# Optimization experiments

Hardware: AMD Instinct MI355X
Metric: run time of the kernel (lower is better)

The kernel has to match this reference:

```python
import jax, jax.numpy as jnp
import numpy as np

N = 50_000      # nodes
E = 800_000     # edges
IN_NF = 16      # input/output node feature dim
H = 64          # hidden_nf
NB = 2          # n_layers (EquivariantBlocks)
NG = 2          # inv_sublayers (GCLs per block)
NORM_FACTOR = 100.0
NORM_CONST = 1.0
EDGE_IN = 2 * H + 2  # edges_in_d = 2 (current + initial squared distance)


def setup_inputs() -> dict:
    key = jax.random.key(0)
    ks = iter(jax.random.split(key, 32))
    rn = lambda s: jax.random.normal(next(ks), s, dtype=jnp.float32)
    lin = lambda s: rn(s) / np.sqrt(s[-2]).astype(np.float32)  # ~xavier-ish
    inp = {
        'h': rn((N, IN_NF)),
        'x': rn((N, 3)),
        'row': jax.random.randint(next(ks), (E,), 0, N, dtype=jnp.int32),
        'col': jax.random.randint(next(ks), (E,), 0, N, dtype=jnp.int32),
        # embedding in/out
        'emb_w': lin((IN_NF, H)), 'emb_b': jnp.zeros((H,), jnp.float32),
        'out_w': lin((H, IN_NF)), 'out_b': jnp.zeros((IN_NF,), jnp.float32),
        # 4 GCLs total (NB*NG), stacked on leading axis
        'e_w1': lin((NB * NG, EDGE_IN, H)), 'e_b1': jnp.zeros((NB * NG, H), jnp.float32),
        'e_w2': lin((NB * NG, H, H)),       'e_b2': jnp.zeros((NB * NG, H), jnp.float32),
        'n_w1': lin((NB * NG, 2 * H, H)),   'n_b1': jnp.zeros((NB * NG, H), jnp.float32),
        'n_w2': lin((NB * NG, H, H)),       'n_b2': jnp.zeros((NB * NG, H), jnp.float32),
        # 2 EquivariantUpdates (one per block)
        'q_w1': lin((NB, EDGE_IN, H)), 'q_b1': jnp.zeros((NB, H), jnp.float32),
        'q_w2': lin((NB, H, H)),       'q_b2': jnp.zeros((NB, H), jnp.float32),
        'q_w3': lin((NB, H, 1)) * 0.001,  # xavier gain=0.001, no bias
    }
    return inp


def _egnn(h, x, row, col, emb_w, emb_b, out_w, out_b,
          e_w1, e_b1, e_w2, e_b2, n_w1, n_b1, n_w2, n_b2,
          q_w1, q_b1, q_w2, q_b2, q_w3):
    def coord2diff(xc):
        d = xc[row] - xc[col]                      # [E,3]
        radial = jnp.sum(d * d, axis=1, keepdims=True)  # [E,1]
        d = d / (jnp.sqrt(radial + 1e-8) + NORM_CONST)
        return radial, d

    dist0, _ = coord2diff(x)                       # initial distances, passed to every block
    h = h @ emb_w + emb_b
    for b in range(NB):
        radial, coord_diff = coord2diff(x)
        edge_attr = jnp.concatenate([radial, dist0], axis=1)  # [E,2]
        for i in range(NG):
            l = b * NG + i
            inp = jnp.concatenate([h[row], h[col], edge_attr], axis=1)  # [E, 2H+2]
            mij = jax.nn.silu(jax.nn.silu(inp @ e_w1[l] + e_b1[l]) @ e_w2[l] + e_b2[l])
            agg = jax.ops.segment_sum(mij, row, num_segments=N) / NORM_FACTOR
            node_in = jnp.concatenate([h, agg], axis=1)                 # [N, 2H]
            h = h + jax.nn.silu(node_in @ n_w1[l] + n_b1[l]) @ n_w2[l] + n_b2[l]
        # equivariant coordinate update
        inp = jnp.concatenate([h[row], h[col], edge_attr], axis=1)
        phi = jax.nn.silu(jax.nn.silu(inp @ q_w1[b] + q_b1[b]) @ q_w2[b] + q_b2[b]) @ q_w3[b]  # [E,1]
        trans = coord_diff * phi
        x = x + jax.ops.segment_sum(trans, row, num_segments=N) / NORM_FACTOR
    h = h @ out_w + out_b
    return h, x


def reference(h, x, row, col, emb_w, emb_b, out_w, out_b,
              e_w1, e_b1, e_w2, e_b2, n_w1, n_b1, n_w2, n_b2,
              q_w1, q_b1, q_w2, q_b2, q_w3):
    return _egnn(h, x, row, col, emb_w, emb_b, out_w, out_b,
                 e_w1, e_b1, e_w2, e_b2, n_w1, n_b1, n_w2, n_b2,
                 q_w1, q_b1, q_w2, q_b2, q_w3)
```

## Files before the change

kernel.cpp:

```cpp
#include <hip/hip_runtime.h>

#define NN 50000
#define NE 800000
#define NB 196

typedef unsigned int  u32;
typedef unsigned short u16;
typedef __attribute__((ext_vector_type(8))) short short8;
typedef __attribute__((ext_vector_type(4))) float f32x4;

union ABfrag { uint2 u2[2]; uint4 u4; short8 s8; };

__device__ __forceinline__ float silu_f(float v) {
    return v * __builtin_amdgcn_rcpf(1.0f + __expf(-v));
}
__device__ __forceinline__ u32 pk2(float lo, float hi) {
    return __builtin_amdgcn_perm(__float_as_uint(hi) + 0x8000u,
                                 __float_as_uint(lo) + 0x8000u, 0x07060302u);
}
__device__ __forceinline__ float bff(u32 h) { return __uint_as_float(h << 16); }

__global__ __launch_bounds__(256, 4) void k_embed(const float* __restrict__ h,
        const float* __restrict__ w, const float* __restrict__ b,
        float* __restrict__ h64) {
    int n = blockIdx.x * 256 + threadIdx.x;
    if (n >= NN) return;
    const float4* h4 = (const float4*)(h + (long)n * 16);
    float in[16];
    #pragma unroll
    for (int c = 0; c < 4; ++c) {
        float4 v = h4[c];
        in[4*c+0] = v.x; in[4*c+1] = v.y; in[4*c+2] = v.z; in[4*c+3] = v.w;
    }
    float acc[64];
    #pragma unroll
    for (int j = 0; j < 64; ++j) acc[j] = b[j];
    #pragma unroll
    for (int k = 0; k < 16; ++k) {
        #pragma unroll
        for (int j = 0; j < 64; ++j) acc[j] = fmaf(in[k], w[k*64 + j], acc[j]);
    }
    float4* o4 = (float4*)(h64 + (long)n * 64);
    #pragma unroll
    for (int c = 0; c < 16; ++c)
        o4[c] = make_float4(acc[4*c+0], acc[4*c+1], acc[4*c+2], acc[4*c+3]);
}

__global__ __launch_bounds__(256, 4) void k_hist(const int* __restrict__ row,
        int* __restrict__ deg) {
    int e = blockIdx.x * 256 + threadIdx.x;
    if (e < NE) atomicAdd(&deg[row[e]], 1);
}

__global__ __launch_bounds__(256, 4) void k_scanA(const int* __restrict__ deg,
        int* __restrict__ bsum) {
    int t = threadIdx.x, i = blockIdx.x * 256 + t;
    int v = (i < NN) ? deg[i] : 0;
    #pragma unroll
    for (int d = 1; d < 64; d <<= 1) v += __shfl_xor(v, d);
    __shared__ int ws[4];
    if ((t & 63) == 0) ws[t >> 6] = v;
    __syncthreads();
    if (t == 0) bsum[blockIdx.x] = ws[0] + ws[1] + ws[2] + ws[3];
}

__global__ __launch_bounds__(256) void k_scanB(const int* __restrict__ bsum,
        int* __restrict__ bpre) {
    __shared__ int s[256];
    int t = threadIdx.x;
    int v = (t < NB) ? bsum[t] : 0;
    s[t] = v;
    __syncthreads();
    #pragma unroll
    for (int d = 1; d < 256; d <<= 1) {
        int u = (t >= d) ? s[t - d] : 0;
        __syncthreads();
        s[t] += u;
        __syncthreads();
    }
    if (t < NB) bpre[t] = s[t] - v;
}

__global__ __launch_bounds__(256, 4) void k_scanC(const int* __restrict__ deg,
        const int* __restrict__ bpre, int* __restrict__ base) {
    int t = threadIdx.x, i = blockIdx.x * 256 + t;
    int lane = t & 63, w = t >> 6;
    int v = (i < NN) ? deg[i] : 0;
    int x = v;
    #pragma unroll
    for (int d = 1; d < 64; d <<= 1) {
        int u = __shfl_up(x, d);
        if (lane >= d) x += u;
    }
    __shared__ int wsum[4];
    if (lane == 63) wsum[w] = x;
    __syncthreads();
    int off = bpre[blockIdx.x];
    #pragma unroll
    for (int ww = 0; ww < 3; ++ww) if (ww < w) off += wsum[ww];
    if (i < NN) base[i] = off + x - v;
}

__global__ __launch_bounds__(256, 4) void k_scatter(const int* __restrict__ row,
        const int* __restrict__ col, int* __restrict__ base,
        int* __restrict__ rowS, int* __restrict__ colS) {
    int e = blockIdx.x * 256 + threadIdx.x;
    if (e >= NE) return;
    int r = row[e];
    int p = atomicAdd(&base[r], 1);
    rowS[p] = r;
    colS[p] = col[e];
}

__global__ __launch_bounds__(256, 4) void k_radial(const float* __restrict__ x,
        const int* __restrict__ rowS, const int* __restrict__ colS,
        float* __restrict__ radial) {
    int e = blockIdx.x * 256 + threadIdx.x;
    if (e >= NE) return;
    int r = rowS[e], c = colS[e];
    float dx = x[r*3+0] - x[c*3+0];
    float dy = x[r*3+1] - x[c*3+1];
    float dz = x[r*3+2] - x[c*3+2];
    radial[e] = dx*dx + dy*dy + dz*dz;
}

__device__ __forceinline__ u32 bfr_rne(float x) {
    u32 u = __float_as_uint(x);
    u += 0x7fffu + ((u >> 16) & 1u);
    return u >> 16;
}
__global__ __launch_bounds__(256, 4) void k_wconv(const float* __restrict__ e_w2,
        const float* __restrict__ q_w2, const float* __restrict__ n_w1,
        const float* __restrict__ n_w2, const float* __restrict__ e_w1,
        const float* __restrict__ q_w1, u16* __restrict__ wf) {
    int t = blockIdx.x * 256 + threadIdx.x;
    if (t >= 122880) return;
    int j, lane, n, s, k, col;
    if (t < 24576) {
        int L = t >> 12, v = t & 4095;
        j = v & 7; lane = (v >> 3) & 63; int ns = v >> 9; n = ns >> 1; s = ns & 1;
        k = 8*(lane >> 4) + j + 32*s;
        col = 16*n + (lane & 15);
        const float* src = (L < 4) ? e_w2 + (size_t)L*4096 : q_w2 + (size_t)(L-4)*4096;
        wf[t] = (u16)bfr_rne(src[k*64 + col]);
    } else if (t < 57344) {
        int u = t - 24576; int L = u >> 13, v = u & 8191;
        j = v & 7; lane = (v >> 3) & 63; int ns = v >> 9; n = ns >> 2; s = ns & 3;
        k = 8*(lane >> 4) + j + 32*s;
        col = 16*n + (lane & 15);
        wf[t] = (u16)bfr_rne(n_w1[(size_t)L*8192 + k*64 + col]);
    } else if (t < 73728) {
        int u = t - 57344; int L = u >> 12, v = u & 4095;
        j = v & 7; lane = (v >> 3) & 63; int ns = v >> 9; n = ns >> 1; s = ns & 1;
        k = 8*(lane >> 4) + j + 32*s;
        col = 16*n + (lane & 15);
        wf[t] = (u16)bfr_rne(n_w2[(size_t)L*4096 + k*64 + col]);
    } else {
        int u = t - 73728;
        int L = u >> 13;
        int v = u & 8191;
        int m = v >> 12;
        int v2 = v & 4095;
        j = v2 & 7; lane = (v2 >> 3) & 63; int ns = v2 >> 9; n = ns >> 1; s = ns & 1;
        k = 8*(lane >> 4) + j + 32*s;
        col = 16*n + (lane & 15);
        const float* src = (L < 4) ? e_w1 + (size_t)L*130*64
                                   : q_w1 + (size_t)(L-4)*130*64;
        wf[t] = (u16)bfr_rne(src[(size_t)(m*64 + k)*64 + col]);
    }
}

__global__ __launch_bounds__(256, 4) void k_pq(const float* __restrict__ h64,
        const u16* __restrict__ wpf, const float* __restrict__ b1,
        u32* __restrict__ Pb, u32* __restrict__ Qb) {
    __shared__ u16 A[64*64];
    __shared__ u16 XP[64*68], XQ[64*68];
    int t = threadIdx.x, w = t >> 6, lane = t & 63;
    int nb0 = blockIdx.x * 64;
    #pragma unroll
    for (int i = 0; i < 4; ++i) {
        int idx = i*256 + t;
        int r = idx >> 4, c = idx & 15;
        int n = nb0 + r;
        float4 v = make_float4(0.f, 0.f, 0.f, 0.f);
        if (n < NN) v = ((const float4*)(h64 + (size_t)n*64))[c];
        uint2 pk = make_uint2(pk2(v.x, v.y), pk2(v.z, v.w));
        *(uint2*)((char*)A + r*128 + ((8*c) ^ ((r & 15) << 3))) = pk;
    }
    __syncthreads();
    int r0 = lane & 15, g = lane >> 4;
    ABfrag bp[2], bq[2];
    #pragma unroll
    for (int s = 0; s < 2; ++s) {
        bp[s].u4 = *(const uint4*)(wpf + ((size_t)(w*2 + s)*64 + lane)*8);
        bq[s].u4 = *(const uint4*)(wpf + 4096 + ((size_t)(w*2 + s)*64 + lane)*8);
    }
    f32x4 aP[4], aQ[4];
    #pragma unroll
    for (int t4 = 0; t4 < 4; ++t4) {
        aP[t4] = (f32x4){0.f, 0.f, 0.f, 0.f};
        aQ[t4] = (f32x4){0.f, 0.f, 0.f, 0.f};
    }
    #pragma unroll
    for (int t4 = 0; t4 < 4; ++t4) {
        #pragma unroll
        for (int s = 0; s < 2; ++s) {
            int boff = 16*g + 64*s;
            ABfrag af;
            af.u2[0] = *(uint2*)((char*)A + (16*t4 + r0)*128 + ( boff      ^ (r0 << 3)));
            af.u2[1] = *(uint2*)((char*)A + (16*t4 + r0)*128 + ((boff + 8) ^ (r0 << 3)));
            aP[t4] = __builtin_amdgcn_mfma_f32_16x16x32_bf16(af.s8, bp[s].s8, aP[t4], 0, 0, 0);
            aQ[t4] = __builtin_amdgcn_mfma_f32_16x16x32_bf16(af.s8, bq[s].s8, aQ[t4], 0, 0, 0);
        }
    }
    float bv = b1[16*w + r0];
    #pragma unroll
    for (int t4 = 0; t4 < 4; ++t4)
        #pragma unroll
        for (int q = 0; q < 4; ++q) {
            int rw = 16*t4 + 4*g + q;
            XP[rw*68 + 16*w + r0] = (u16)(pk2(aP[t4][q] + bv, 0.f) & 0xffffu);
            XQ[rw*68 + 16*w + r0] = (u16)(pk2(aQ[t4][q], 0.f) & 0xffffu);
        }
    __syncthreads();
    int node = t >> 2, part = t & 3;
    if (nb0 + node < NN) {
        const u32* XPw = (const u32*)XP;
        const u32* XQw = (const u32*)XQ;
        u32 b[8];
        #pragma unroll
        for (int j = 0; j < 8; ++j) b[j] = XPw[node*34 + 8*part + j];
        uint4* dp = (uint4*)(Pb + (size_t)(nb0 + node)*32 + part*8);
        dp[0] = make_uint4(b[0], b[1], b[2], b[3]);
        dp[1] = make_uint4(b[4], b[5], b[6], b[7]);
        #pragma unroll
        for (int j = 0; j < 8; ++j) b[j] = XQw[node*34 + 8*part + j];
        uint4* dq = (uint4*)(Qb + (size_t)(nb0 + node)*32 + part*8);
        dq[0] = make_uint4(b[0], b[1], b[2], b[3]);
        dq[1] = make_uint4(b[4], b[5], b[6], b[7]);
    }
}

__global__ __launch_bounds__(256, 4) void k_edge(
        const u32* __restrict__ Pb, const u32* __restrict__ Qb,
        const float* __restrict__ radial, const float* __restrict__ dist0,
        const int* __restrict__ rowS, const int* __restrict__ colS,
        const float* __restrict__ w1t, const u16* __restrict__ w2f,
        const float* __restrict__ b2, float* __restrict__ agg) {
    __shared__ u16 S_lds[4][4224];
    int tid = threadIdx.x;
    int w = tid >> 6, lane = tid & 63;
    int e = blockIdx.x * 256 + w * 64 + lane;
    u16* Aw = S_lds[w];
    int r = rowS[e], c = colS[e];
    float rad = radial[e], d0 = dist0[e];
    const uint4* Pr = (const uint4*)(Pb + (size_t)r * 32);
    const uint4* Qc = (const uint4*)(Qb + (size_t)c * 32);
    int swz = (lane & 15) << 3;
    #pragma unroll
    for (int c8 = 0; c8 < 8; ++c8) {
        uint4 pu = Pr[c8], qu = Qc[c8];
        u32 pw[4] = {pu.x, pu.y, pu.z, pu.w};
        u32 qw[4] = {qu.x, qu.y, qu.z, qu.w};
        float hv[8];
        #pragma unroll
        for (int k2 = 0; k2 < 4; ++k2) {
            int f = 8*c8 + 2*k2;
            float pl = bff(pw[k2] & 0xffffu), ph = bff(pw[k2] >> 16);
            float ql = bff(qw[k2] & 0xffffu), qh = bff(qw[k2] >> 16);
            hv[2*k2]   = silu_f(pl + ql + rad*w1t[f]     + d0*w1t[64+f]);
            hv[2*k2+1] = silu_f(ph + qh + rad*w1t[f+1]   + d0*w1t[64+f+1]);
        }
        uint2 pkA = make_uint2(pk2(hv[0], hv[1]), pk2(hv[2], hv[3]));
        uint2 pkB = make_uint2(pk2(hv[4], hv[5]), pk2(hv[6], hv[7]));
        *(uint2*)((char*)Aw + lane*128 + ((16*c8)     ^ swz)) = pkA;
        *(uint2*)((char*)Aw + lane*128 + ((16*c8 + 8) ^ swz)) = pkB;
    }
    __syncthreads();
    ABfrag bf[4][2];
    #pragma unroll
    for (int n = 0; n < 4; ++n)
        #pragma unroll
        for (int s = 0; s < 2; ++s)
            bf[n][s].u4 = *(const uint4*)(w2f + ((n*2 + s)*64 + lane)*8);
    int r0 = lane & 15, g = lane >> 4;
    f32x4 acc[4][4];
    #pragma unroll
    for (int t = 0; t < 4; ++t)
        #pragma unroll
        for (int n = 0; n < 4; ++n)
            acc[t][n] = (f32x4){0.f, 0.f, 0.f, 0.f};
    #pragma unroll
    for (int t = 0; t < 4; ++t) {
        #pragma unroll
        for (int s = 0; s < 2; ++s) {
            int boff = 16*g + 64*s;
            ABfrag af;
            af.u2[0] = *(uint2*)((char*)Aw + (16*t + r0)*128 + ( boff      ^ (r0 << 3)));
            af.u2[1] = *(uint2*)((char*)Aw + (16*t + r0)*128 + ((boff + 8) ^ (r0 << 3)));
            #pragma unroll
            for (int n = 0; n < 4; ++n)
                acc[t][n] = __builtin_amdgcn_mfma_f32_16x16x32_bf16(
                    af.s8, bf[n][s].s8, acc[t][n], 0, 0, 0);
        }
    }
    __syncthreads();
    u16* Mw = Aw;
    #pragma unroll
    for (int n = 0; n < 4; ++n) {
        float b2v = b2[16*n + r0];
        #pragma unroll
        for (int t = 0; t < 4; ++t) {
            f32x4 z = acc[t][n];
            u32 p0 = pk2(silu_f(z[0] + b2v), silu_f(z[1] + b2v));
            u32 p1 = pk2(silu_f(z[2] + b2v), silu_f(z[3] + b2v));
            *(uint2*)((char*)Mw + (16*n + r0)*132 + 32*t + 8*g) = make_uint2(p0, p1);
        }
    }
    __syncthreads();
    int rnext = __shfl_down(r, 1);
    unsigned long long tm = __ballot((lane == 63) || (rnext != r));
    float racc = 0.0f;
    #pragma unroll
    for (int ch = 0; ch < 16; ++ch) {
        uint2 mm = *(uint2*)((char*)Mw + lane*132 + 8*ch);
        u32 mw[2] = {mm.x, mm.y};
        #pragma unroll
        for (int q = 0; q < 4; ++q) {
            int ee = 4*ch + q;
            racc += bff((mw[q >> 1] >> ((q & 1) * 16)) & 0xffffu);
            if ((tm >> ee) & 1ull) {
                int rr = __builtin_amdgcn_readlane(r, ee);
                atomicAdd(&agg[(size_t)rr*64 + lane], racc);
                racc = 0.0f;
            }
        }
    }
}

__global__ __launch_bounds__(256, 3) void k_node_pq(float* __restrict__ h64,
        const float* __restrict__ agg,
        const u16* __restrict__ w1f, const float* __restrict__ b1,
        const u16* __restrict__ w2f, const float* __restrict__ b2,
        const u16* __restrict__ wpf, const float* __restrict__ b1pq,
        u32* __restrict__ Pb, u32* __restrict__ Qb) {
    __shared__ u16 S[16512];
    u16* A0 = S;
    u16* A1 = S + 4096;
    u16* H  = S + 8192;
    u16* D  = S + 12288;
    u16* An = S;
    u16* XPh = S + 4096;
    u16* XQh = S + 8448;
    int t = threadIdx.x, w = t >> 6, lane = t & 63;
    int nb0 = blockIdx.x * 64;
    #pragma unroll
    for (int i = 0; i < 8; ++i) {
        int idx = i*256 + t;
        int r = idx >> 5, c = idx & 31;
        int n = nb0 + r;
        float4 v = make_float4(0.f, 0.f, 0.f, 0.f);
        if (n < NN) {
            if (c < 16) v = ((const float4*)(h64 + (size_t)n*64))[c];
            else {
                float4 a = ((const float4*)(agg + (size_t)n*64))[c-16];
                v = make_float4(a.x*0.01f, a.y*0.01f, a.z*0.01f, a.w*0.01f);
            }
        }
        uint2 pk = make_uint2(pk2(v.x, v.y), pk2(v.z, v.w));
        u16* dst = (c < 16) ? A0 : A1;
        int cc = c & 15;
        *(uint2*)((char*)dst + r*128 + ((8*cc) ^ ((r & 15) << 3))) = pk;
    }
    __syncthreads();
    int r0 = lane & 15, g = lane >> 4;
    ABfrag bf1[4];
    #pragma unroll
    for (int s = 0; s < 4; ++s)
        bf1[s].u4 = *(const uint4*)(w1f + ((size_t)(w*4 + s)*64 + lane)*8);
    f32x4 acc[4];
    #pragma unroll
    for (int t4 = 0; t4 < 4; ++t4) acc[t4] = (f32x4){0.f, 0.f, 0.f, 0.f};
    #pragma unroll
    for (int t4 = 0; t4 < 4; ++t4) {
        #pragma unroll
        for (int s = 0; s < 4; ++s) {
            const u16* Ah = (s < 2) ? A0 : A1;
            int boff = 16*g + 64*(s & 1);
            ABfrag af;
            af.u2[0] = *(uint2*)((char*)Ah + (16*t4 + r0)*128 + ( boff      ^ (r0 << 3)));
            af.u2[1] = *(uint2*)((char*)Ah + (16*t4 + r0)*128 + ((boff + 8) ^ (r0 << 3)));
            acc[t4] = __builtin_amdgcn_mfma_f32_16x16x32_bf16(
                af.s8, bf1[s].s8, acc[t4], 0, 0, 0);
        }
    }
    float b1v = b1[16*w + r0];
    #pragma unroll
    for (int t4 = 0; t4 < 4; ++t4)
        #pragma unroll
        for (int q = 0; q < 4; ++q) {
            int rw = 16*t4 + 4*g + q;
            u16 hv = (u16)(pk2(silu_f(acc[t4][q] + b1v), 0.f) & 0xffffu);
            *(u16*)((char*)H + rw*128 + ((2*(16*w + r0)) ^ ((rw & 15) << 3))) = hv;
        }
    __syncthreads();
    ABfrag bf2[2];
    #pragma unroll
    for (int s = 0; s < 2; ++s)
        bf2[s].u4 = *(const uint4*)(w2f + ((size_t)(w*2 + s)*64 + lane)*8);
    f32x4 acc2[4];
    #pragma unroll
    for (int t4 = 0; t4 < 4; ++t4) acc2[t4] = (f32x4){0.f, 0.f, 0.f, 0.f};
    #pragma unroll
    for (int t4 = 0; t4 < 4; ++t4) {
        #pragma unroll
        for (int s = 0; s < 2; ++s) {
            int boff = 16*g + 64*s;
            ABfrag af;
            af.u2[0] = *(uint2*)((char*)H + (16*t4 + r0)*128 + ( boff      ^ (r0 << 3)));
            af.u2[1] = *(uint2*)((char*)H + (16*t4 + r0)*128 + ((boff + 8) ^ (r0 << 3)));
            acc2[t4] = __builtin_amdgcn_mfma_f32_16x16x32_bf16(
                af.s8, bf2[s].s8, acc2[t4], 0, 0, 0);
        }
    }
    float b2v = b2[16*w + r0];
    #pragma unroll
    for (int t4 = 0; t4 < 4; ++t4)
        #pragma unroll
        for (int q = 0; q < 4; ++q) {
            int rw = 16*t4 + 4*g + q;
            D[rw*66 + 16*w + r0] = (u16)(pk2(acc2[t4][q] + b2v, 0.f) & 0xffffu);
        }
    __syncthreads();
    #pragma unroll
    for (int i = 0; i < 4; ++i) {
        int idx = i*256 + t;
        int rr = idx >> 4, cc = idx & 15;
        int n = nb0 + rr;
        float4 v = make_float4(0.f, 0.f, 0.f, 0.f);
        if (n < NN) {
            v = ((const float4*)(h64 + (size_t)n*64))[cc];
            v.x += bff(D[rr*66 + 4*cc + 0]);
            v.y += bff(D[rr*66 + 4*cc + 1]);
            v.z += bff(D[rr*66 + 4*cc + 2]);
            v.w += bff(D[rr*66 + 4*cc + 3]);
            ((float4*)(h64 + (size_t)n*64))[cc] = v;
        }
        uint2 pk = make_uint2(pk2(v.x, v.y), pk2(v.z, v.w));
        *(uint2*)((char*)An + rr*128 + ((8*cc) ^ ((rr & 15) << 3))) = pk;
    }
    __syncthreads();
    ABfrag bp[2], bq[2];
    #pragma unroll
    for (int s = 0; s < 2; ++s) {
        bp[s].u4 = *(const uint4*)(wpf + ((size_t)(w*2 + s)*64 + lane)*8);
        bq[s].u4 = *(const uint4*)(wpf + 4096 + ((size_t)(w*2 + s)*64 + lane)*8);
    }
    f32x4 aP[4], aQ[4];
    #pragma unroll
    for (int t4 = 0; t4 < 4; ++t4) {
        aP[t4] = (f32x4){0.f, 0.f, 0.f, 0.f};
        aQ[t4] = (f32x4){0.f, 0.f, 0.f, 0.f};
    }
    #pragma unroll
    for (int t4 = 0; t4 < 4; ++t4) {
        #pragma unroll
        for (int s = 0; s < 2; ++s) {
            int boff = 16*g + 64*s;
            ABfrag af;
            af.u2[0] = *(uint2*)((char*)An + (16*t4 + r0)*128 + ( boff      ^ (r0 << 3)));
            af.u2[1] = *(uint2*)((char*)An + (16*t4 + r0)*128 + ((boff + 8) ^ (r0 << 3)));
            aP[t4] = __builtin_amdgcn_mfma_f32_16x16x32_bf16(af.s8, bp[s].s8, aP[t4], 0, 0, 0);
            aQ[t4] = __builtin_amdgcn_mfma_f32_16x16x32_bf16(af.s8, bq[s].s8, aQ[t4], 0, 0, 0);
        }
    }
    float bv = b1pq[16*w + r0];
    #pragma unroll
    for (int t4 = 0; t4 < 4; ++t4)
        #pragma unroll
        for (int q = 0; q < 4; ++q) {
            int rw = 16*t4 + 4*g + q;
            XPh[rw*68 + 16*w + r0] = (u16)(pk2(aP[t4][q] + bv, 0.f) & 0xffffu);
            XQh[rw*68 + 16*w + r0] = (u16)(pk2(aQ[t4][q], 0.f) & 0xffffu);
        }
    __syncthreads();
    int node = t >> 2, part = t & 3;
    if (nb0 + node < NN) {
        const u32* XPw = (const u32*)XPh;
        const u32* XQw = (const u32*)XQh;
        u32 b[8];
        #pragma unroll
        for (int j = 0; j < 8; ++j) b[j] = XPw[node*34 + 8*part + j];
        uint4* dp = (uint4*)(Pb + (size_t)(nb0 + node)*32 + part*8);
        dp[0] = make_uint4(b[0], b[1], b[2], b[3]);
        dp[1] = make_uint4(b[4], b[5], b[6], b[7]);
        #pragma unroll
        for (int j = 0; j < 8; ++j) b[j] = XQw[node*34 + 8*part + j];
        uint4* dq = (uint4*)(Qb + (size_t)(nb0 + node)*32 + part*8);
        dq[0] = make_uint4(b[0], b[1], b[2], b[3]);
        dq[1] = make_uint4(b[4], b[5], b[6], b[7]);
    }
}

__global__ __launch_bounds__(256, 4) void k_coord(
        const u32* __restrict__ Pb, const u32* __restrict__ Qb,
        const float* __restrict__ radial, const float* __restrict__ dist0,
        const int* __restrict__ rowS, const int* __restrict__ colS,
        const float* __restrict__ w1t, const u16* __restrict__ w2f,
        const float* __restrict__ b2, const float* __restrict__ w3,
        const float* __restrict__ x_old, float* __restrict__ x_new) {
    __shared__ u16 A_lds[4][4096];
    int tid = threadIdx.x;
    int w = tid >> 6, lane = tid & 63;
    int e = blockIdx.x * 256 + w * 64 + lane;
    u16* Aw = A_lds[w];
    int r = rowS[e], c = colS[e];
    float rad = radial[e], d0 = dist0[e];
    const uint4* Pr = (const uint4*)(Pb + (size_t)r * 32);
    const uint4* Qc = (const uint4*)(Qb + (size_t)c * 32);
    int swz = (lane & 15) << 3;
    #pragma unroll
    for (int c8 = 0; c8 < 8; ++c8) {
        uint4 pu = Pr[c8], qu = Qc[c8];
        u32 pw[4] = {pu.x, pu.y, pu.z, pu.w};
        u32 qw[4] = {qu.x, qu.y, qu.z, qu.w};
        float hv[8];
        #pragma unroll
        for (int k2 = 0; k2 < 4; ++k2) {
            int f = 8*c8 + 2*k2;
            float pl = bff(pw[k2] & 0xffffu), ph = bff(pw[k2] >> 16);
            float ql = bff(qw[k2] & 0xffffu), qh = bff(qw[k2] >> 16);
            hv[2*k2]   = silu_f(pl + ql + rad*w1t[f]   + d0*w1t[64+f]);
            hv[2*k2+1] = silu_f(ph + qh + rad*w1t[f+1] + d0*w1t[64+f+1]);
        }
        uint2 pkA = make_uint2(pk2(hv[0], hv[1]), pk2(hv[2], hv[3]));
        uint2 pkB = make_uint2(pk2(hv[4], hv[5]), pk2(hv[6], hv[7]));
        *(uint2*)((char*)Aw + lane*128 + ((16*c8)     ^ swz)) = pkA;
        *(uint2*)((char*)Aw + lane*128 + ((16*c8 + 8) ^ swz)) = pkB;
    }
    __syncthreads();
    ABfrag bf[4][2];
    #pragma unroll
    for (int n = 0; n < 4; ++n)
        #pragma unroll
        for (int s = 0; s < 2; ++s)
            bf[n][s].u4 = *(const uint4*)(w2f + ((n*2 + s)*64 + lane)*8);
    int r0 = lane & 15, g = lane >> 4;
    f32x4 acc[4][4];
    #pragma unroll
    for (int t = 0; t < 4; ++t)
        #pragma unroll
        for (int n = 0; n < 4; ++n)
            acc[t][n] = (f32x4){0.f, 0.f, 0.f, 0.f};
    #pragma unroll
    for (int t = 0; t < 4; ++t) {
        #pragma unroll
        for (int s = 0; s < 2; ++s) {
            int boff = 16*g + 64*s;
            ABfrag af;
            af.u2[0] = *(uint2*)((char*)Aw + (16*t + r0)*128 + ( boff      ^ (r0 << 3)));
            af.u2[1] = *(uint2*)((char*)Aw + (16*t + r0)*128 + ((boff + 8) ^ (r0 << 3)));
            #pragma unroll
            for (int n = 0; n < 4; ++n)
                acc[t][n] = __builtin_amdgcn_mfma_f32_16x16x32_bf16(
                    af.s8, bf[n][s].s8, acc[t][n], 0, 0, 0);
        }
    }
    float w3v[4], b2v[4];
    #pragma unroll
    for (int n = 0; n < 4; ++n) { w3v[n] = w3[16*n + r0]; b2v[n] = b2[16*n + r0]; }
    float ph[16];
    #pragma unroll
    for (int t = 0; t < 4; ++t)
        #pragma unroll
        for (int q = 0; q < 4; ++q) {
            float s = 0.f;
            #pragma unroll
            for (int n = 0; n < 4; ++n)
                s = fmaf(silu_f(acc[t][n][q] + b2v[n]), w3v[n], s);
            ph[t*4 + q] = s;
        }
    __syncthreads();
    float* Mw = (float*)Aw;
    #pragma unroll
    for (int t4 = 0; t4 < 4; ++t4)
        #pragma unroll
        for (int q = 0; q < 4; ++q)
            Mw[(16*t4 + 4*g + q)*17 + r0] = ph[t4*4 + q];
    __syncthreads();
    float phi = 0.f;
    #pragma unroll
    for (int i = 0; i < 16; ++i) phi += Mw[lane*17 + i];
    phi *= 0.01f;
    float dx = x_old[r*3+0] - x_old[c*3+0];
    float dy = x_old[r*3+1] - x_old[c*3+1];
    float dz = x_old[r*3+2] - x_old[c*3+2];
    float inv = phi / (sqrtf(rad + 1e-8f) + 1.0f);
    float tx = dx * inv, ty = dy * inv, tz = dz * inv;
    int rprev = __shfl_up(r, 1);
    bool head = (lane == 0) || (rprev != r);
    unsigned long long hm = __ballot(head);
    int runid = __popcll(hm & ((2ull << lane) - 1ull));
    #pragma unroll
    for (int d = 1; d < 64; d <<= 1) {
        float ox = __shfl_up(tx, d);
        float oy = __shfl_up(ty, d);
        float oz = __shfl_up(tz, d);
        int orid = __shfl_up(runid, d);
        if (lane >= d && orid == runid) { tx += ox; ty += oy; tz += oz; }
    }
    int rid_next = __shfl_down(runid, 1);
    bool tail = (lane == 63) || (rid_next != runid);
    if (tail) {
        atomicAdd(&x_new[r*3+0], tx);
        atomicAdd(&x_new[r*3+1], ty);
        atomicAdd(&x_new[r*3+2], tz);
    }
}

__global__ __launch_bounds__(256, 4) void k_out(const float* __restrict__ h64,
        const float* __restrict__ w, const float* __restrict__ b,
        float* __restrict__ out) {
    int n = blockIdx.x * 256 + threadIdx.x;
    if (n >= NN) return;
    float acc[16];
    #pragma unroll
    for (int j = 0; j < 16; ++j) acc[j] = b[j];
    const float4* h4 = (const float4*)(h64 + (long)n*64);
    #pragma unroll
    for (int c = 0; c < 16; ++c) {
        float4 v = h4[c];
        float vv[4] = {v.x, v.y, v.z, v.w};
        #pragma unroll
        for (int t = 0; t < 4; ++t) {
            #pragma unroll
            for (int j = 0; j < 16; ++j)
                acc[j] = fmaf(vv[t], w[(4*c+t)*16 + j], acc[j]);
        }
    }
    float4* o4 = (float4*)(out + (long)n*16);
    #pragma unroll
    for (int cq = 0; cq < 4; ++cq)
        o4[cq] = make_float4(acc[4*cq+0],acc[4*cq+1],acc[4*cq+2],acc[4*cq+3]);
}

extern "C" void kernel_launch(void* const* d_in, const int* in_sizes, int n_in,
                              void* d_out, int out_size, void* d_ws, size_t ws_size,
                              hipStream_t stream) {
    const float* h_in  = (const float*)d_in[0];
    const float* x_in  = (const float*)d_in[1];
    const int*   row   = (const int*)d_in[2];
    const int*   col   = (const int*)d_in[3];
    const float* emb_w = (const float*)d_in[4];
    const float* emb_b = (const float*)d_in[5];
    const float* out_w = (const float*)d_in[6];
    const float* out_b = (const float*)d_in[7];
    const float* e_w1  = (const float*)d_in[8];
    const float* e_b1  = (const float*)d_in[9];
    const float* e_w2  = (const float*)d_in[10];
    const float* e_b2  = (const float*)d_in[11];
    const float* n_w1  = (const float*)d_in[12];
    const float* n_b1  = (const float*)d_in[13];
    const float* n_w2  = (const float*)d_in[14];
    const float* n_b2  = (const float*)d_in[15];
    const float* q_w1  = (const float*)d_in[16];
    const float* q_b1  = (const float*)d_in[17];
    const float* q_w2  = (const float*)d_in[18];
    const float* q_b2  = (const float*)d_in[19];
    const float* q_w3  = (const float*)d_in[20];

    const size_t WF_N = 122880;
    const size_t WF_BYTES = WF_N * sizeof(u16);
    size_t need = WF_BYTES + ((size_t)NN*64*4 + (size_t)NE*2 + (size_t)NN*3
                   + (size_t)NE*2 + (size_t)NN*2 + 1024) * sizeof(float);
    if (ws_size < need) return;

    u16*   wf    = (u16*)d_ws;
    float* fb    = (float*)((char*)d_ws + WF_BYTES);
    float* h64   = fb;
    u32*   Pb    = (u32*)(h64 + (size_t)NN*64);
    u32*   Qb    = Pb + (size_t)NN*32;
    float* agg   = (float*)(Qb + (size_t)NN*32);
    float* d0S   = agg   + (size_t)NN*64;
    float* radS  = d0S   + (size_t)NE;
    float* xA    = radS  + (size_t)NE;
    int*   rowS  = (int*)(xA + (size_t)NN*3);
    int*   colS  = rowS  + (size_t)NE;
    int*   deg   = colS  + (size_t)NE;
    int*   base  = deg   + (size_t)NN;
    int*   bsum  = base  + (size_t)NN;
    int*   bpre  = bsum  + 256;

    float* out_h = (float*)d_out;
    float* out_x = out_h + (size_t)NN*16;

    dim3 th(256);
    dim3 nb((NN + 255)/256);
    dim3 eb(NE/256);
    dim3 t64b((NN + 63)/64);

    hipMemsetAsync(deg, 0, (size_t)NN*sizeof(int), stream);
    k_hist<<<eb, th, 0, stream>>>(row, deg);
    k_scanA<<<NB, th, 0, stream>>>(deg, bsum);
    k_scanB<<<1, th, 0, stream>>>(bsum, bpre);
    k_scanC<<<NB, th, 0, stream>>>(deg, bpre, base);
    k_scatter<<<eb, th, 0, stream>>>(row, col, base, rowS, colS);
    k_wconv<<<480, th, 0, stream>>>(e_w2, q_w2, n_w1, n_w2, e_w1, q_w1, wf);

    k_radial<<<eb, th, 0, stream>>>(x_in, rowS, colS, d0S);
    k_embed<<<nb, th, 0, stream>>>(h_in, emb_w, emb_b, h64);

    const u16* nw1f = wf + 24576;
    const u16* nw2f = wf + 57344;
    const u16* pqf  = wf + 73728;

    for (int b = 0; b < 2; ++b) {
        const float* x_old;
        float*       x_new;
        const float* radp;
        if (b == 0) {
            x_old = x_in;  x_new = xA;    radp = d0S;
        } else {
            x_old = xA;    x_new = out_x; radp = radS;
            k_radial<<<eb, th, 0, stream>>>(x_old, rowS, colS, radS);
        }
        for (int i = 0; i < 2; ++i) {
            int l = b*2 + i;
            if (i == 0)
                k_pq<<<t64b, th, 0, stream>>>(h64, pqf + (size_t)l*8192,
                                              e_b1 + (size_t)l*64, Pb, Qb);
            hipMemsetAsync(agg, 0, (size_t)NN*64*sizeof(float), stream);
            k_edge<<<eb, th, 0, stream>>>(Pb, Qb, radp, d0S, rowS, colS,
                    e_w1 + (size_t)l*130*64 + 128*64,
                    wf + (size_t)l*4096,
                    e_b2 + (size_t)l*64, agg);
            const u16* nxt_f  = (i == 0) ? pqf + (size_t)(l+1)*8192
                                         : pqf + (size_t)(4 + b)*8192;
            const float* nxt_b = (i == 0) ? e_b1 + (size_t)(l+1)*64
                                          : q_b1 + (size_t)b*64;
            k_node_pq<<<t64b, th, 0, stream>>>(h64, agg,
                    nw1f + (size_t)l*8192, n_b1 + (size_t)l*64,
                    nw2f + (size_t)l*4096, n_b2 + (size_t)l*64,
                    nxt_f, nxt_b, Pb, Qb);
        }
        hipMemcpyAsync(x_new, x_old, (size_t)NN*3*sizeof(float),
                       hipMemcpyDeviceToDevice, stream);
        k_coord<<<eb, th, 0, stream>>>(Pb, Qb, radp, d0S, rowS, colS,
                q_w1 + (size_t)b*130*64 + 128*64,
                wf + (size_t)(4 + b)*4096,
                q_b2 + (size_t)b*64, q_w3 + (size_t)b*64, x_old, x_new);
    }
    k_out<<<nb, th, 0, stream>>>(h64, out_w, out_b, out_h);
}
```

Measured before the change: 655.8 us.

## Build MFMA A-fragments directly from gathered node features, skip LDS staging

```diff
diff --git a/kernel.cpp b/kernel.cpp
--- a/kernel.cpp
+++ b/kernel.cpp
@@ -247,79 +247,73 @@
         const int* __restrict__ rowS, const int* __restrict__ colS,
         const float* __restrict__ w1t, const u16* __restrict__ w2f,
         const float* __restrict__ b2, float* __restrict__ agg) {
-    __shared__ u16 S_lds[4][4224];
+    __shared__ u16 M_lds[4][64*66];
     int tid = threadIdx.x;
     int w = tid >> 6, lane = tid & 63;
-    int e = blockIdx.x * 256 + w * 64 + lane;
-    u16* Aw = S_lds[w];
-    int r = rowS[e], c = colS[e];
-    float rad = radial[e], d0 = dist0[e];
-    const uint4* Pr = (const uint4*)(Pb + (size_t)r * 32);
-    const uint4* Qc = (const uint4*)(Qb + (size_t)c * 32);
-    int swz = (lane & 15) << 3;
-    #pragma unroll
-    for (int c8 = 0; c8 < 8; ++c8) {
-        uint4 pu = Pr[c8], qu = Qc[c8];
-        u32 pw[4] = {pu.x, pu.y, pu.z, pu.w};
-        u32 qw[4] = {qu.x, qu.y, qu.z, qu.w};
-        float hv[8];
-        #pragma unroll
-        for (int k2 = 0; k2 < 4; ++k2) {
-            int f = 8*c8 + 2*k2;
-            float pl = bff(pw[k2] & 0xffffu), ph = bff(pw[k2] >> 16);
-            float ql = bff(qw[k2] & 0xffffu), qh = bff(qw[k2] >> 16);
-            hv[2*k2]   = silu_f(pl + ql + rad*w1t[f]     + d0*w1t[64+f]);
-            hv[2*k2+1] = silu_f(ph + qh + rad*w1t[f+1]   + d0*w1t[64+f+1]);
-        }
-        uint2 pkA = make_uint2(pk2(hv[0], hv[1]), pk2(hv[2], hv[3]));
-        uint2 pkB = make_uint2(pk2(hv[4], hv[5]), pk2(hv[6], hv[7]));
-        *(uint2*)((char*)Aw + lane*128 + ((16*c8)     ^ swz)) = pkA;
-        *(uint2*)((char*)Aw + lane*128 + ((16*c8 + 8) ^ swz)) = pkB;
-    }
-    __syncthreads();
+    int ebase = blockIdx.x * 256 + w * 64;
+    u16* Mw = M_lds[w];
+    int r0 = lane & 15, g = lane >> 4;
+    float wa[16], wb[16];
+    *(float4*)&wa[0]  = *(const float4*)(w1t + 8*g);
+    *(float4*)&wa[4]  = *(const float4*)(w1t + 8*g + 4);
+    *(float4*)&wa[8]  = *(const float4*)(w1t + 32 + 8*g);
+    *(float4*)&wa[12] = *(const float4*)(w1t + 36 + 8*g);
+    *(float4*)&wb[0]  = *(const float4*)(w1t + 64 + 8*g);
+    *(float4*)&wb[4]  = *(const float4*)(w1t + 68 + 8*g);
+    *(float4*)&wb[8]  = *(const float4*)(w1t + 96 + 8*g);
+    *(float4*)&wb[12] = *(const float4*)(w1t + 100 + 8*g);
     ABfrag bf[4][2];
     #pragma unroll
     for (int n = 0; n < 4; ++n)
         #pragma unroll
         for (int s = 0; s < 2; ++s)
             bf[n][s].u4 = *(const uint4*)(w2f + ((n*2 + s)*64 + lane)*8);
-    int r0 = lane & 15, g = lane >> 4;
-    f32x4 acc[4][4];
-    #pragma unroll
-    for (int t = 0; t < 4; ++t)
-        #pragma unroll
-        for (int n = 0; n < 4; ++n)
-            acc[t][n] = (f32x4){0.f, 0.f, 0.f, 0.f};
+    float b2v[4];
+    #pragma unroll
+    for (int n = 0; n < 4; ++n) b2v[n] = b2[16*n + r0];
     #pragma unroll
     for (int t = 0; t < 4; ++t) {
-        #pragma unroll
-        for (int s = 0; s < 2; ++s) {
-            int boff = 16*g + 64*s;
-            ABfrag af;
-            af.u2[0] = *(uint2*)((char*)Aw + (16*t + r0)*128 + ( boff      ^ (r0 << 3)));
-            af.u2[1] = *(uint2*)((char*)Aw + (16*t + r0)*128 + ((boff + 8) ^ (r0 << 3)));
-            #pragma unroll
-            for (int n = 0; n < 4; ++n)
-                acc[t][n] = __builtin_amdgcn_mfma_f32_16x16x32_bf16(
-                    af.s8, bf[n][s].s8, acc[t][n], 0, 0, 0);
-        }
-    }
-    __syncthreads();
-    u16* Mw = Aw;
-    #pragma unroll
-    for (int n = 0; n < 4; ++n) {
-        float b2v = b2[16*n + r0];
-        #pragma unroll
-        for (int t = 0; t < 4; ++t) {
-            f32x4 z = acc[t][n];
-            u32 p0 = pk2(silu_f(z[0] + b2v), silu_f(z[1] + b2v));
-            u32 p1 = pk2(silu_f(z[2] + b2v), silu_f(z[3] + b2v));
-            *(uint2*)((char*)Mw + (16*n + r0)*132 + 32*t + 8*g) = make_uint2(p0, p1);
-        }
-    }
-    __syncthreads();
-    int rnext = __shfl_down(r, 1);
-    unsigned long long tm = __ballot((lane == 63) || (rnext != r));
+        int et = ebase + 16*t + r0;
+        int r = rowS[et], c = colS[et];
+        float rad = radial[et], d0 = dist0[et];
+        uint4 pA = *(const uint4*)(Pb + (size_t)r*32 + 4*g);
+        uint4 pB = *(const uint4*)(Pb + (size_t)r*32 + 16 + 4*g);
+        uint4 qA = *(const uint4*)(Qb + (size_t)c*32 + 4*g);
+        uint4 qB = *(const uint4*)(Qb + (size_t)c*32 + 16 + 4*g);
+        u32 pu[8] = {pA.x, pA.y, pA.z, pA.w, pB.x, pB.y, pB.z, pB.w};
+        u32 qu[8] = {qA.x, qA.y, qA.z, qA.w, qB.x, qB.y, qB.z, qB.w};
+        u32 pk[8];
+        #pragma unroll
+        for (int i = 0; i < 8; ++i) {
+            int kb = (i >> 2) * 8 + (i & 3) * 2;
+            float pl = bff(pu[i] & 0xffffu), ph = bff(pu[i] >> 16);
+            float ql = bff(qu[i] & 0xffffu), qh = bff(qu[i] >> 16);
+            float h0 = silu_f(pl + ql + rad*wa[kb]   + d0*wb[kb]);
+            float h1 = silu_f(ph + qh + rad*wa[kb+1] + d0*wb[kb+1]);
+            pk[i] = pk2(h0, h1);
+        }
+        ABfrag af0, af1;
+        af0.u4 = make_uint4(pk[0], pk[1], pk[2], pk[3]);
+        af1.u4 = make_uint4(pk[4], pk[5], pk[6], pk[7]);
+        f32x4 acc[4];
+        #pragma unroll
+        for (int n = 0; n < 4; ++n) acc[n] = (f32x4){0.f, 0.f, 0.f, 0.f};
+        #pragma unroll
+        for (int n = 0; n < 4; ++n) {
+            acc[n] = __builtin_amdgcn_mfma_f32_16x16x32_bf16(af0.s8, bf[n][0].s8, acc[n], 0, 0, 0);
+            acc[n] = __builtin_amdgcn_mfma_f32_16x16x32_bf16(af1.s8, bf[n][1].s8, acc[n], 0, 0, 0);
+        }
+        #pragma unroll
+        for (int n = 0; n < 4; ++n) {
+            f32x4 z = acc[n];
+            u32 m0 = pk2(silu_f(z[0] + b2v[n]), silu_f(z[1] + b2v[n]));
+            u32 m1 = pk2(silu_f(z[2] + b2v[n]), silu_f(z[3] + b2v[n]));
+            *(uint2*)((char*)Mw + (16*n + r0)*132 + 32*t + 8*g) = make_uint2(m0, m1);
+        }
+    }
+    int rl = rowS[ebase + lane];
+    int rnext = __shfl_down(rl, 1);
+    unsigned long long tm = __ballot((lane == 63) || (rnext != rl));
     float racc = 0.0f;
     #pragma unroll
     for (int ch = 0; ch < 16; ++ch) {
@@ -330,7 +324,7 @@
             int ee = 4*ch + q;
             racc += bff((mw[q >> 1] >> ((q & 1) * 16)) & 0xffffu);
             if ((tm >> ee) & 1ull) {
-                int rr = __builtin_amdgcn_readlane(r, ee);
+                int rr = __builtin_amdgcn_readlane(rl, ee);
                 atomicAdd(&agg[(size_t)rr*64 + lane], racc);
                 racc = 0.0f;
             }
@@ -509,89 +503,86 @@
         const float* __restrict__ w1t, const u16* __restrict__ w2f,
         const float* __restrict__ b2, const float* __restrict__ w3,
         const float* __restrict__ x_old, float* __restrict__ x_new) {
-    __shared__ u16 A_lds[4][4096];
+    __shared__ float PHL[4][64];
     int tid = threadIdx.x;
     int w = tid >> 6, lane = tid & 63;
-    int e = blockIdx.x * 256 + w * 64 + lane;
-    u16* Aw = A_lds[w];
-    int r = rowS[e], c = colS[e];
-    float rad = radial[e], d0 = dist0[e];
-    const uint4* Pr = (const uint4*)(Pb + (size_t)r * 32);
-    const uint4* Qc = (const uint4*)(Qb + (size_t)c * 32);
-    int swz = (lane & 15) << 3;
-    #pragma unroll
-    for (int c8 = 0; c8 < 8; ++c8) {
-        uint4 pu = Pr[c8], qu = Qc[c8];
-        u32 pw[4] = {pu.x, pu.y, pu.z, pu.w};
-        u32 qw[4] = {qu.x, qu.y, qu.z, qu.w};
-        float hv[8];
-        #pragma unroll
-        for (int k2 = 0; k2 < 4; ++k2) {
-            int f = 8*c8 + 2*k2;
-            float pl = bff(pw[k2] & 0xffffu), ph = bff(pw[k2] >> 16);
-            float ql = bff(qw[k2] & 0xffffu), qh = bff(qw[k2] >> 16);
-            hv[2*k2]   = silu_f(pl + ql + rad*w1t[f]   + d0*w1t[64+f]);
-            hv[2*k2+1] = silu_f(ph + qh + rad*w1t[f+1] + d0*w1t[64+f+1]);
-        }
-        uint2 pkA = make_uint2(pk2(hv[0], hv[1]), pk2(hv[2], hv[3]));
-        uint2 pkB = make_uint2(pk2(hv[4], hv[5]), pk2(hv[6], hv[7]));
-        *(uint2*)((char*)Aw + lane*128 + ((16*c8)     ^ swz)) = pkA;
-        *(uint2*)((char*)Aw + lane*128 + ((16*c8 + 8) ^ swz)) = pkB;
-    }
-    __syncthreads();
+    int ebase = blockIdx.x * 256 + w * 64;
+    int r0 = lane & 15, g = lane >> 4;
+    float wa[16], wb[16];
+    *(float4*)&wa[0]  = *(const float4*)(w1t + 8*g);
+    *(float4*)&wa[4]  = *(const float4*)(w1t + 8*g + 4);
+    *(float4*)&wa[8]  = *(const float4*)(w1t + 32 + 8*g);
+    *(float4*)&wa[12] = *(const float4*)(w1t + 36 + 8*g);
+    *(float4*)&wb[0]  = *(const float4*)(w1t + 64 + 8*g);
+    *(float4*)&wb[4]  = *(const float4*)(w1t + 68 + 8*g);
+    *(float4*)&wb[8]  = *(const float4*)(w1t + 96 + 8*g);
+    *(float4*)&wb[12] = *(const float4*)(w1t + 100 + 8*g);
     ABfrag bf[4][2];
     #pragma unroll
     for (int n = 0; n < 4; ++n)
         #pragma unroll
         for (int s = 0; s < 2; ++s)
             bf[n][s].u4 = *(const uint4*)(w2f + ((n*2 + s)*64 + lane)*8);
-    int r0 = lane & 15, g = lane >> 4;
-    f32x4 acc[4][4];
-    #pragma unroll
-    for (int t = 0; t < 4; ++t)
-        #pragma unroll
-        for (int n = 0; n < 4; ++n)
-            acc[t][n] = (f32x4){0.f, 0.f, 0.f, 0.f};
-    #pragma unroll
-    for (int t = 0; t < 4; ++t) {
-        #pragma unroll
-        for (int s = 0; s < 2; ++s) {
-            int boff = 16*g + 64*s;
-            ABfrag af;
-            af.u2[0] = *(uint2*)((char*)Aw + (16*t + r0)*128 + ( boff      ^ (r0 << 3)));
-            af.u2[1] = *(uint2*)((char*)Aw + (16*t + r0)*128 + ((boff + 8) ^ (r0 << 3)));
-            #pragma unroll
-            for (int n = 0; n < 4; ++n)
-                acc[t][n] = __builtin_amdgcn_mfma_f32_16x16x32_bf16(
-                    af.s8, bf[n][s].s8, acc[t][n], 0, 0, 0);
-        }
-    }
     float w3v[4], b2v[4];
     #pragma unroll
     for (int n = 0; n < 4; ++n) { w3v[n] = w3[16*n + r0]; b2v[n] = b2[16*n + r0]; }
     float ph[16];
     #pragma unroll
-    for (int t = 0; t < 4; ++t)
+    for (int t = 0; t < 4; ++t) {
+        int et = ebase + 16*t + r0;
+        int r = rowS[et], c = colS[et];
+        float rad = radial[et], d0 = dist0[et];
+        uint4 pA = *(const uint4*)(Pb + (size_t)r*32 + 4*g);
+        uint4 pB = *(const uint4*)(Pb + (size_t)r*32 + 16 + 4*g);
+        uint4 qA = *(const uint4*)(Qb + (size_t)c*32 + 4*g);
+        uint4 qB = *(const uint4*)(Qb + (size_t)c*32 + 16 + 4*g);
+        u32 pu[8] = {pA.x, pA.y, pA.z, pA.w, pB.x, pB.y, pB.z, pB.w};
+        u32 qu[8] = {qA.x, qA.y, qA.z, qA.w, qB.x, qB.y, qB.z, qB.w};
+        u32 pk[8];
+        #pragma unroll
+        for (int i = 0; i < 8; ++i) {
+            int kb = (i >> 2) * 8 + (i & 3) * 2;
+            float pl = bff(pu[i] & 0xffffu), phh = bff(pu[i] >> 16);
+            float ql = bff(qu[i] & 0xffffu), qh = bff(qu[i] >> 16);
+            float h0 = silu_f(pl + ql + rad*wa[kb]   + d0*wb[kb]);
+            float h1 = silu_f(phh + qh + rad*wa[kb+1] + d0*wb[kb+1]);
+            pk[i] = pk2(h0, h1);
+        }
+        ABfrag af0, af1;
+        af0.u4 = make_uint4(pk[0], pk[1], pk[2], pk[3]);
+        af1.u4 = make_uint4(pk[4], pk[5], pk[6], pk[7]);
+        f32x4 acc[4];
+        #pragma unroll
+        for (int n = 0; n < 4; ++n) acc[n] = (f32x4){0.f, 0.f, 0.f, 0.f};
+        #pragma unroll
+        for (int n = 0; n < 4; ++n) {
+            acc[n] = __builtin_amdgcn_mfma_f32_16x16x32_bf16(af0.s8, bf[n][0].s8, acc[n], 0, 0, 0);
+            acc[n] = __builtin_amdgcn_mfma_f32_16x16x32_bf16(af1.s8, bf[n][1].s8, acc[n], 0, 0, 0);
+        }
         #pragma unroll
         for (int q = 0; q < 4; ++q) {
             float s = 0.f;
             #pragma unroll
             for (int n = 0; n < 4; ++n)
-                s = fmaf(silu_f(acc[t][n][q] + b2v[n]), w3v[n], s);
+                s = fmaf(silu_f(acc[n][q] + b2v[n]), w3v[n], s);
             ph[t*4 + q] = s;
         }
-    __syncthreads();
-    float* Mw = (float*)Aw;
-    #pragma unroll
-    for (int t4 = 0; t4 < 4; ++t4)
-        #pragma unroll
-        for (int q = 0; q < 4; ++q)
-            Mw[(16*t4 + 4*g + q)*17 + r0] = ph[t4*4 + q];
-    __syncthreads();
-    float phi = 0.f;
-    #pragma unroll
-    for (int i = 0; i < 16; ++i) phi += Mw[lane*17 + i];
-    phi *= 0.01f;
+    }
+    #pragma unroll
+    for (int d = 1; d < 16; d <<= 1)
+        #pragma unroll
+        for (int i = 0; i < 16; ++i) ph[i] += __shfl_xor(ph[i], d);
+    if (r0 == 0) {
+        #pragma unroll
+        for (int t = 0; t < 4; ++t)
+            #pragma unroll
+            for (int q = 0; q < 4; ++q)
+                PHL[w][16*t + 4*g + q] = ph[t*4 + q];
+    }
+    int e = ebase + lane;
+    float phi = PHL[w][lane] * 0.01f;
+    int r = rowS[e], c = colS[e];
+    float rad = radial[e];
     float dx = x_old[r*3+0] - x_old[c*3+0];
     float dy = x_old[r*3+1] - x_old[c*3+1];
     float dz = x_old[r*3+2] - x_old[c*3+2];
```

Measured after the change: 668.8 us. About the same (+2.0%).
